# Kernel optimization log

Hardware: AMD Instinct MI355X
Metric: run time of the kernel (lower is better)

## Reference

```python
import jax, jax.numpy as jnp
import numpy as np

# ---- static config (matches init_kwargs / langevin args) ----
B, N, D = 2, 16384, 3
F_DIM = 128      # feature_net.out_channels
H_DIM = 128      # score_net hidden
N_BLOCKS = 2
K = 4            # denoise_knn
NUM_STEPS = 4
STEP_SIZE = 0.2
STEP_DECAY = 0.95

# static sliding-window neighbor indices, computed once (numpy -> constant)
_offsets = np.arange(-(K - 1) // 2, (K - 1) // 2 + 1)
NBR_IDX = np.clip(np.arange(N)[:, None] + _offsets, 0, N - 1)   # (N, K)
NBR_FLAT = NBR_IDX.reshape(-1)                                  # (N*K,)


def setup_inputs() -> dict:
    key = jax.random.key(0)
    ks = jax.random.split(key, 8)
    s = 0.05
    return {
        "pcl_noisy": jax.random.normal(ks[0], (B, N, D), jnp.float32),
        "Wf1": jax.random.normal(ks[1], (D, F_DIM), jnp.float32) * s,
        "bf1": jnp.zeros((F_DIM,), jnp.float32),
        "Wf2": jax.random.normal(ks[2], (F_DIM, F_DIM), jnp.float32) * s,
        "bf2": jnp.zeros((F_DIM,), jnp.float32),
        "W0": jax.random.normal(ks[3], (D + F_DIM, H_DIM), jnp.float32) * s,
        "b0": jnp.zeros((H_DIM,), jnp.float32),
        "Wb": jax.random.normal(ks[4], (N_BLOCKS, H_DIM, H_DIM), jnp.float32) * s,
        "bb": jnp.zeros((N_BLOCKS, H_DIM), jnp.float32),
        "Wo": jax.random.normal(ks[5], (H_DIM, D), jnp.float32) * s,
        "bo": jnp.zeros((D,), jnp.float32),
    }


def _feature_net(pcl, Wf1, bf1, Wf2, bf2):
    # pointwise MLP: (B,N,3) -> (B,N,F)
    h = jax.nn.relu(pcl @ Wf1 + bf1)
    return h @ Wf2 + bf2


def _score_net(x_cent, feat, W0, b0, Wb, bb, Wo, bo):
    # x_cent: (B,N,K,3) centered frames, feat: (B,N,F) per-seed context
    c = jnp.broadcast_to(feat[:, :, None, :], x_cent.shape[:3] + (feat.shape[-1],))
    h = jax.nn.relu(jnp.concatenate([x_cent, c], axis=-1) @ W0 + b0)  # (B,N,K,H)
    for i in range(N_BLOCKS):  # small fixed residual stack
        h = h + jax.nn.relu(h @ Wb[i] + bb[i])
    return h @ Wo + bo  # (B,N,K,3)


def reference(pcl_noisy, Wf1, bf1, Wf2, bf2, W0, b0, Wb, bb, Wo, bo):
    feat = _feature_net(pcl_noisy, Wf1, bf1, Wf2, bf2)  # (B,N,F), computed once

    def step(pcl_next, step_i):
        frames = pcl_next[:, NBR_IDX, :]                      # gather (B,N,K,3)
        centered = frames - pcl_noisy[:, :, None, :]          # center on original cloud
        grad_pred = _score_net(centered, feat, W0, b0, Wb, bb, Wo, bo)  # (B,N,K,3)
        acc = jnp.zeros_like(pcl_noisy).at[:, NBR_FLAT, :].add(
            grad_pred.reshape(pcl_noisy.shape[0], -1, D))     # scatter_add (B,N,3)
        s = STEP_SIZE * (STEP_DECAY ** step_i.astype(jnp.float32))
        return pcl_next + s * acc, None

    pcl_next, _ = jax.lax.scan(step, pcl_noisy, jnp.arange(NUM_STEPS))
    return pcl_next
```

## Files before the change

### kernel.cpp

```cpp
#include <hip/hip_runtime.h>
#include <hip/hip_bf16.h>

#define NPT    16384
#define TOTP   32768
#define FD     128
#define CHK    64
#define CPB    (NPT/CHK)
#define GRID   (2*CPB)
#define EXT    (CHK+24)
#define FQM    (CHK+21)

#define OFF_WFA 0
#define OFF_WFB 16384
#define OFF_WB  32768
#define OFF_WO  98304
#define PREP_TOT 100352

typedef unsigned short u16;
typedef __attribute__((ext_vector_type(8))) short bf16x8;
typedef __attribute__((ext_vector_type(4))) float f32x4;

__device__ __forceinline__ float bf2f(u16 u) {
    union { unsigned int i; float f; } v; v.i = ((unsigned int)u) << 16; return v.f;
}
__device__ __forceinline__ u16 f2bf(float f) {
    union { float f; unsigned int i; } v; v.f = f;
    unsigned int u = v.i;
    u = u + 0x7FFFu + ((u >> 16) & 1u);
    return (u16)(u >> 16);
}
__device__ __forceinline__ u16 f2bf_hw(float f) {
    __hip_bfloat16 h = __float2bfloat16(f);
    return *(u16*)&h;
}
__device__ __forceinline__ int swz(int row, int colbyte) {
    return row*256 + (colbyte ^ ((row & 7) << 4));
}
__device__ __forceinline__ int fswz(int row, int col) {
    return row*256 + ((col*2) ^ ((row & 7) << 4));
}

__global__ __launch_bounds__(256) void prep_weights(
    const float* __restrict__ Wf2, const float* __restrict__ W0,
    const float* __restrict__ Wb,  const float* __restrict__ Wo,
    u16* __restrict__ W)
{
    int t = blockIdx.x*256 + threadIdx.x;
    if (t >= PREP_TOT) return;
    float val;
    if (t < OFF_WB) {
        int u = t & 16383;
        int e = u & 7, l = (u >> 3) & 63, kk = (u >> 9) & 3;
        int ntg = (u >> 11) & 1, wid = (u >> 12) & 3;
        int col = wid*32 + ntg*16 + (l & 15);
        int k   = kk*32 + (l >> 4)*8 + e;
        val = (t < OFF_WFB) ? Wf2[k*FD + col] : W0[(3+k)*FD + col];
    } else if (t < OFF_WO) {
        int u = t - OFF_WB;
        int e = u & 7, l = (u >> 3) & 63, kk = (u >> 9) & 3;
        int ntg = (u >> 11) & 1, layer = (u >> 12) & 1, wid = (u >> 13) & 3;
        int col = wid*32 + ntg*16 + (l & 15);
        int k   = kk*32 + (l >> 4)*8 + e;
        val = Wb[layer*FD*FD + k*FD + col];
    } else {
        int u = t - OFF_WO;
        int e = u & 7, l = (u >> 3) & 63, kk = (u >> 9) & 3;
        int l15 = l & 15;
        int k   = kk*32 + (l >> 4)*8 + e;
        val = (l15 < 3) ? Wo[k*3 + l15] : 0.f;
    }
    W[t] = f2bf(val);
}

__global__ __launch_bounds__(256, 2) void fused_all(
    const float* __restrict__ pcl, const float* __restrict__ Wf1,
    const float* __restrict__ bf1, const float* __restrict__ bf2,
    const float* __restrict__ W0,  const float* __restrict__ b0,
    const float* __restrict__ bb,  const float* __restrict__ bo,
    const u16* __restrict__ Wprep, float* __restrict__ out)
{
    __shared__ __align__(16) u16   fpl[FQM*128];
    __shared__ __align__(16) float X0l[EXT*3];
    __shared__ __align__(16) float Xal[EXT*3];
    __shared__ __align__(16) float Xbl[EXT*3];
    __shared__ __align__(16) char  hA0[8192];
    __shared__ __align__(16) char  hA1[8192];
    __shared__ __align__(16) char  hB0[8192];
    __shared__ __align__(16) char  hB1[8192];
    __shared__ __align__(16) char  hC0[8192];
    __shared__ __align__(16) char  hC1[8192];

    const int tid = threadIdx.x, wid = tid >> 6, l = tid & 63;
    const int l15 = l & 15, l4 = l >> 4;
    const int colb = wid * 32;

    const int blk = blockIdx.x;
    const int b = blk >> 8, cidx = blk & (CPB - 1);
    const int A = cidx * CHK;
    const int Bp = A + CHK - 1;
    const int elo  = (A - 12 < 0) ? 0 : A - 12;
    const int ehi  = (Bp + 12 > NPT-1) ? NPT-1 : Bp + 12;
    const int esz3 = (ehi - elo + 1) * 3;
    const int fqlo = (A - 10 < 0) ? 0 : A - 10;
    const int fqhi = (Bp + 11 > NPT-1) ? NPT-1 : Bp + 11;
    const int fqc  = fqhi - fqlo + 1;
    const size_t gb = (size_t)b * NPT;

    for (int i = tid; i < esz3; i += 256) X0l[i] = pcl[(gb + elo)*3 + i];
    __syncthreads();

    {
        bf16x8 wfA[2][4], wfB[2][4];
        {
            const bf16x8* fa = (const bf16x8*)(Wprep + OFF_WFA);
            const bf16x8* fb = (const bf16x8*)(Wprep + OFF_WFB);
            #pragma unroll
            for (int ntg = 0; ntg < 2; ++ntg)
                #pragma unroll
                for (int kk = 0; kk < 4; ++kk) {
                    int fi = ((wid*2 + ntg)*4 + kk)*64 + l;
                    wfA[ntg][kk] = fa[fi];
                    wfB[ntg][kk] = fb[fi];
                }
        }
        float wf1c[3][2], bf1v[2], bf2v[2], b0v[2];
        #pragma unroll
        for (int ntg = 0; ntg < 2; ++ntg) {
            int col = colb + ntg*16 + l15;
            wf1c[0][ntg] = Wf1[0*FD+col];
            wf1c[1][ntg] = Wf1[1*FD+col];
            wf1c[2][ntg] = Wf1[2*FD+col];
            bf1v[ntg] = bf1[col]; bf2v[ntg] = bf2[col]; b0v[ntg] = b0[col];
        }
        const int nft = (fqc + 31) >> 5;
        for (int ft = 0; ft < nft; ++ft) {
            const int r0 = ft*32;
            #pragma unroll
            for (int rt = 0; rt < 2; ++rt)
                #pragma unroll
                for (int reg = 0; reg < 4; ++reg) {
                    int row = rt*16 + l4*4 + reg;
                    int q = fqlo + r0 + row; if (q > fqhi) q = fqhi;
                    int qe = (q - elo)*3;
                    float px = X0l[qe], py = X0l[qe+1], pz = X0l[qe+2];
                    #pragma unroll
                    for (int ntg = 0; ntg < 2; ++ntg) {
                        float tv = bf1v[ntg] + px*wf1c[0][ntg] + py*wf1c[1][ntg] + pz*wf1c[2][ntg];
                        tv = fmaxf(tv, 0.f);
                        int col = colb + ntg*16 + l15;
                        *(u16*)(hA0 + swz(row, col*2)) = f2bf_hw(tv);
                    }
                }
            __syncthreads();
            {
                bf16x8 a[2][4];
                #pragma unroll
                for (int rt = 0; rt < 2; ++rt)
                    #pragma unroll
                    for (int kk = 0; kk < 4; ++kk)
                        a[rt][kk] = *(const bf16x8*)(hA0 + swz(rt*16 + l15, kk*64 + l4*16));
                #pragma unroll
                for (int ntg = 0; ntg < 2; ++ntg) {
                    f32x4 acc0 = {bf2v[ntg],bf2v[ntg],bf2v[ntg],bf2v[ntg]};
                    f32x4 acc1 = acc0;
                    #pragma unroll
                    for (int kk = 0; kk < 4; ++kk) {
                        acc0 = __builtin_amdgcn_mfma_f32_16x16x32_bf16(a[0][kk], wfA[ntg][kk], acc0, 0,0,0);
                        acc1 = __builtin_amdgcn_mfma_f32_16x16x32_bf16(a[1][kk], wfA[ntg][kk], acc1, 0,0,0);
                    }
                    int col = colb + ntg*16 + l15;
                    #pragma unroll
                    for (int reg = 0; reg < 4; ++reg) {
                        *(u16*)(hB0 + swz(l4*4+reg,    col*2)) = f2bf_hw(acc0[reg]);
                        *(u16*)(hB0 + swz(16+l4*4+reg, col*2)) = f2bf_hw(acc1[reg]);
                    }
                }
            }
            __syncthreads();
            {
                bf16x8 a[2][4];
                #pragma unroll
                for (int rt = 0; rt < 2; ++rt)
                    #pragma unroll
                    for (int kk = 0; kk < 4; ++kk)
                        a[rt][kk] = *(const bf16x8*)(hB0 + swz(rt*16 + l15, kk*64 + l4*16));
                #pragma unroll
                for (int ntg = 0; ntg < 2; ++ntg) {
                    f32x4 acc0 = {b0v[ntg],b0v[ntg],b0v[ntg],b0v[ntg]};
                    f32x4 acc1 = acc0;
                    #pragma unroll
                    for (int kk = 0; kk < 4; ++kk) {
                        acc0 = __builtin_amdgcn_mfma_f32_16x16x32_bf16(a[0][kk], wfB[ntg][kk], acc0, 0,0,0);
                        acc1 = __builtin_amdgcn_mfma_f32_16x16x32_bf16(a[1][kk], wfB[ntg][kk], acc1, 0,0,0);
                    }
                    int col = colb + ntg*16 + l15;
                    #pragma unroll
                    for (int reg = 0; reg < 4; ++reg) {
                        int ra = r0 + l4*4 + reg, rb = r0 + 16 + l4*4 + reg;
                        if (ra < fqc) *(u16*)((char*)fpl + fswz(ra, col)) = f2bf_hw(acc0[reg]);
                        if (rb < fqc) *(u16*)((char*)fpl + fswz(rb, col)) = f2bf_hw(acc1[reg]);
                    }
                }
            }
            __syncthreads();
        }
    }
    __builtin_amdgcn_sched_barrier(0);

    bf16x8 wfrag[2][2][4], wofrag[4];
    {
        const bf16x8* wb = (const bf16x8*)(Wprep + OFF_WB);
        #pragma unroll
        for (int layer = 0; layer < 2; ++layer)
            #pragma unroll
            for (int ntg = 0; ntg < 2; ++ntg)
                #pragma unroll
                for (int kk = 0; kk < 4; ++kk)
                    wfrag[layer][ntg][kk] = wb[(((wid*2+layer)*2+ntg)*4+kk)*64 + l];
        const bf16x8* wo = (const bf16x8*)(Wprep + OFF_WO);
        #pragma unroll
        for (int kk = 0; kk < 4; ++kk) wofrag[kk] = wo[kk*64 + l];
    }
    float w0c[3][2], bbv[2][2];
    #pragma unroll
    for (int ntg = 0; ntg < 2; ++ntg) {
        int col = colb + ntg*16 + l15;
        w0c[0][ntg] = W0[0*FD+col];
        w0c[1][ntg] = W0[1*FD+col];
        w0c[2][ntg] = W0[2*FD+col];
        bbv[0][ntg] = bb[col]; bbv[1][ntg] = bb[FD+col];
    }
    const float bol = (l15 < 3) ? bo[l15] : 0.f;

    auto do_step = [&](const float* curl, float* nxtl, float sval, int qlo, int qhi) {
        for (int i = tid; i < esz3; i += 256) nxtl[i] = curl[i];
        __syncthreads();

        auto layer0 = [&](char* hAt, int qbase, float (&hc)[2][2][4]) {
            #pragma unroll
            for (int rt = 0; rt < 2; ++rt) {
                int q = qbase + rt*4 + l4; if (q > qhi) q = qhi;
                int qe = (q - elo)*3;
                float nx = X0l[qe], ny = X0l[qe+1], nz = X0l[qe+2];
                float cx[4], cy[4], cz[4];
                #pragma unroll
                for (int k = 0; k < 4; ++k) {
                    int nb = q + k - 2;
                    nb = nb < 0 ? 0 : (nb > NPT-1 ? NPT-1 : nb);
                    int te = (nb - elo)*3;
                    cx[k] = curl[te]   - nx;
                    cy[k] = curl[te+1] - ny;
                    cz[k] = curl[te+2] - nz;
                }
                #pragma unroll
                for (int ntg = 0; ntg < 2; ++ntg) {
                    int col = colb + ntg*16 + l15;
                    float fp = bf2f(*(const u16*)((const char*)fpl + fswz(q - fqlo, col)));
                    #pragma unroll
                    for (int reg = 0; reg < 4; ++reg) {
                        float u = fp + cx[reg]*w0c[0][ntg] + cy[reg]*w0c[1][ntg] + cz[reg]*w0c[2][ntg];
                        u = fmaxf(u, 0.f);
                        hc[rt][ntg][reg] = u;
                        *(u16*)(hAt + swz(rt*16 + l4*4 + reg, col*2)) = f2bf_hw(u);
                    }
                }
            }
        };
        auto layer1 = [&](const char* hAt, char* hBt, float (&hc)[2][2][4]) {
            bf16x8 a[2][4];
            #pragma unroll
            for (int rt = 0; rt < 2; ++rt)
                #pragma unroll
                for (int kk = 0; kk < 4; ++kk)
                    a[rt][kk] = *(const bf16x8*)(hAt + swz(rt*16 + l15, kk*64 + l4*16));
            #pragma unroll
            for (int ntg = 0; ntg < 2; ++ntg) {
                f32x4 acc0 = {bbv[0][ntg],bbv[0][ntg],bbv[0][ntg],bbv[0][ntg]};
                f32x4 acc1 = acc0;
                #pragma unroll
                for (int kk = 0; kk < 4; ++kk) {
                    acc0 = __builtin_amdgcn_mfma_f32_16x16x32_bf16(a[0][kk], wfrag[0][ntg][kk], acc0, 0,0,0);
                    acc1 = __builtin_amdgcn_mfma_f32_16x16x32_bf16(a[1][kk], wfrag[0][ntg][kk], acc1, 0,0,0);
                }
                int col = colb + ntg*16 + l15;
                #pragma unroll
                for (int reg = 0; reg < 4; ++reg) {
                    hc[0][ntg][reg] += fmaxf(acc0[reg], 0.f);
                    hc[1][ntg][reg] += fmaxf(acc1[reg], 0.f);
                    *(u16*)(hBt + swz(l4*4+reg,    col*2)) = f2bf_hw(hc[0][ntg][reg]);
                    *(u16*)(hBt + swz(16+l4*4+reg, col*2)) = f2bf_hw(hc[1][ntg][reg]);
                }
            }
        };
        auto layer2 = [&](const char* hBt, char* hCt, float (&hc)[2][2][4]) {
            bf16x8 a[2][4];
            #pragma unroll
            for (int rt = 0; rt < 2; ++rt)
                #pragma unroll
                for (int kk = 0; kk < 4; ++kk)
                    a[rt][kk] = *(const bf16x8*)(hBt + swz(rt*16 + l15, kk*64 + l4*16));
            #pragma unroll
            for (int ntg = 0; ntg < 2; ++ntg) {
                f32x4 acc0 = {bbv[1][ntg],bbv[1][ntg],bbv[1][ntg],bbv[1][ntg]};
                f32x4 acc1 = acc0;
                #pragma unroll
                for (int kk = 0; kk < 4; ++kk) {
                    acc0 = __builtin_amdgcn_mfma_f32_16x16x32_bf16(a[0][kk], wfrag[1][ntg][kk], acc0, 0,0,0);
                    acc1 = __builtin_amdgcn_mfma_f32_16x16x32_bf16(a[1][kk], wfrag[1][ntg][kk], acc1, 0,0,0);
                }
                int col = colb + ntg*16 + l15;
                #pragma unroll
                for (int reg = 0; reg < 4; ++reg) {
                    float h0 = hc[0][ntg][reg] + fmaxf(acc0[reg], 0.f);
                    float h1 = hc[1][ntg][reg] + fmaxf(acc1[reg], 0.f);
                    *(u16*)(hCt + swz(l4*4+reg,    col*2)) = f2bf_hw(h0);
                    *(u16*)(hCt + swz(16+l4*4+reg, col*2)) = f2bf_hw(h1);
                }
            }
        };

        const int nt_ = (qhi - qlo + 8) >> 3;
        const int ng_ = (nt_ + 1) >> 1;
        for (int g = 0; g < ng_; ++g) {
            const int qb0 = qlo + (g*2)*8;
            const int qb1 = qlo + (g*2+1)*8;
            const bool has1 = (g*2+1) < nt_;
            float hc0[2][2][4], hc1[2][2][4];
            layer0(hA0, qb0, hc0);
            if (has1) layer0(hA1, qb1, hc1);
            __syncthreads();
            layer1(hA0, hB0, hc0);
            if (has1) layer1(hA1, hB1, hc1);
            __syncthreads();
            layer2(hB0, hC0, hc0);
            if (has1) layer2(hB1, hC1, hc1);
            __syncthreads();
            {
                const int t = wid >> 1, sub = wid & 1;
                const char* hCt = t ? hC1 : hC0;
                const int qb = t ? qb1 : qb0;
                bf16x8 a[4];
                #pragma unroll
                for (int kk = 0; kk < 4; ++kk)
                    a[kk] = *(const bf16x8*)(hCt + swz(sub*16 + l15, kk*64 + l4*16));
                f32x4 acc = {0.f,0.f,0.f,0.f};
                #pragma unroll
                for (int kk = 0; kk < 4; ++kk)
                    acc = __builtin_amdgcn_mfma_f32_16x16x32_bf16(a[kk], wofrag[kk], acc, 0,0,0);
                int q = qb + sub*4 + l4;
                if (l15 < 3 && q <= qhi) {
                    #pragma unroll
                    for (int reg = 0; reg < 4; ++reg) {
                        int nb = q + reg - 2;
                        nb = nb < 0 ? 0 : (nb > NPT-1 ? NPT-1 : nb);
                        atomicAdd(&nxtl[(nb - elo)*3 + l15], sval*(acc[reg] + bol));
                    }
                }
            }
        }
        __syncthreads();
    };

    const int q1lo = fqlo,                 q1hi = fqhi;
    const int q2lo = (A-7 < 0) ? 0 : A-7,  q2hi = (Bp+8 > NPT-1) ? NPT-1 : Bp+8;
    const int q3lo = (A-4 < 0) ? 0 : A-4,  q3hi = (Bp+5 > NPT-1) ? NPT-1 : Bp+5;
    const int q4lo = (A-1 < 0) ? 0 : A-1,  q4hi = (Bp+2 > NPT-1) ? NPT-1 : Bp+2;

    do_step(X0l, Xal, 0.2f,      q1lo, q1hi);
    do_step(Xal, Xbl, 0.19f,     q2lo, q2hi);
    do_step(Xbl, Xal, 0.1805f,   q3lo, q3hi);
    do_step(Xal, Xbl, 0.171475f, q4lo, q4hi);

    for (int i = tid; i < CHK*3; i += 256)
        out[(gb + A)*3 + i] = Xbl[(A - elo)*3 + i];
}

extern "C" void kernel_launch(void* const* d_in, const int* in_sizes, int n_in,
                              void* d_out, int out_size, void* d_ws, size_t ws_size,
                              hipStream_t stream) {
    const float* pcl = (const float*)d_in[0];
    const float* Wf1 = (const float*)d_in[1];
    const float* bf1 = (const float*)d_in[2];
    const float* Wf2 = (const float*)d_in[3];
    const float* bf2 = (const float*)d_in[4];
    const float* W0  = (const float*)d_in[5];
    const float* b0  = (const float*)d_in[6];
    const float* Wb  = (const float*)d_in[7];
    const float* bb  = (const float*)d_in[8];
    const float* Wo  = (const float*)d_in[9];
    const float* bo  = (const float*)d_in[10];
    float* out = (float*)d_out;

    u16* Wprep = (u16*)d_ws;

    prep_weights<<<(PREP_TOT+255)/256, 256, 0, stream>>>(Wf2, W0, Wb, Wo, Wprep);
    fused_all<<<GRID, 256, 0, stream>>>(pcl, Wf1, bf1, bf2, W0, b0, bb, bo, Wprep, out);
}
```

Before: 174.5 us.

## Interleave activation tiles as packed bf16 pairs and pad point coords to float4

Changes the LDS activation layout so each 32-bit word holds the values for row r and row r+16, which lets each layer write packed u32 stores instead of 16-bit stores. Reads do two 16-byte loads followed by bit shuffles that rebuild the MFMA A fragments. Point-cloud buffers in LDS are padded to four floats per point so neighbour and center reads, step copies and atomics use float4 accesses. The aim is fewer, wider LDS transactions, at the cost of extra ALU work to unpack fragments and somewhat more LDS for coordinates.

Result: slower. 237.2 us (+35.9%).

```diff
diff --git a/kernel.cpp b/kernel.cpp
--- a/kernel.cpp
+++ b/kernel.cpp
@@ -17,6 +17,7 @@
 #define PREP_TOT 100352
 
 typedef unsigned short u16;
+typedef unsigned int   u32;
 typedef __attribute__((ext_vector_type(8))) short bf16x8;
 typedef __attribute__((ext_vector_type(4))) float f32x4;
 
@@ -33,8 +34,11 @@
     __hip_bfloat16 h = __float2bfloat16(f);
     return *(u16*)&h;
 }
-__device__ __forceinline__ int swz(int row, int colbyte) {
-    return row*256 + (colbyte ^ ((row & 7) << 4));
+__device__ __forceinline__ u32 pk2(float lo, float hi) {
+    return (u32)f2bf_hw(lo) | ((u32)f2bf_hw(hi) << 16);
+}
+__device__ __forceinline__ int hswz(int r15, int col) {
+    return r15*512 + ((col*4) ^ ((r15 & 7) << 4));
 }
 __device__ __forceinline__ int fswz(int row, int col) {
     return row*256 + ((col*2) ^ ((row & 7) << 4));
@@ -80,9 +84,9 @@
     const u16* __restrict__ Wprep, float* __restrict__ out)
 {
     __shared__ __align__(16) u16   fpl[FQM*128];
-    __shared__ __align__(16) float X0l[EXT*3];
-    __shared__ __align__(16) float Xal[EXT*3];
-    __shared__ __align__(16) float Xbl[EXT*3];
+    __shared__ __align__(16) float X0l[EXT*4];
+    __shared__ __align__(16) float Xal[EXT*4];
+    __shared__ __align__(16) float Xbl[EXT*4];
     __shared__ __align__(16) char  hA0[8192];
     __shared__ __align__(16) char  hA1[8192];
     __shared__ __align__(16) char  hB0[8192];
@@ -100,14 +104,41 @@
     const int Bp = A + CHK - 1;
     const int elo  = (A - 12 < 0) ? 0 : A - 12;
     const int ehi  = (Bp + 12 > NPT-1) ? NPT-1 : Bp + 12;
-    const int esz3 = (ehi - elo + 1) * 3;
+    const int extc = ehi - elo + 1;
     const int fqlo = (A - 10 < 0) ? 0 : A - 10;
     const int fqhi = (Bp + 11 > NPT-1) ? NPT-1 : Bp + 11;
     const int fqc  = fqhi - fqlo + 1;
     const size_t gb = (size_t)b * NPT;
 
-    for (int i = tid; i < esz3; i += 256) X0l[i] = pcl[(gb + elo)*3 + i];
+    for (int i = tid; i < extc; i += 256) {
+        float4 v;
+        v.x = pcl[(gb + elo + i)*3 + 0];
+        v.y = pcl[(gb + elo + i)*3 + 1];
+        v.z = pcl[(gb + elo + i)*3 + 2];
+        v.w = 0.f;
+        *(float4*)&X0l[i*4] = v;
+    }
     __syncthreads();
+
+    auto load_ab = [&](const char* hXt, bf16x8 (&a)[2][4]) {
+        #pragma unroll
+        for (int kk = 0; kk < 4; ++kk) {
+            int k0 = kk*32 + l4*8;
+            uint4 da = *(const uint4*)(hXt + hswz(l15, k0));
+            uint4 db = *(const uint4*)(hXt + hswz(l15, k0 + 4));
+            union { u32 u[4]; bf16x8 v; } u0, u1;
+            u0.u[0] = (da.x & 0xffffu) | (da.y << 16);
+            u0.u[1] = (da.z & 0xffffu) | (da.w << 16);
+            u0.u[2] = (db.x & 0xffffu) | (db.y << 16);
+            u0.u[3] = (db.z & 0xffffu) | (db.w << 16);
+            u1.u[0] = (da.x >> 16) | (da.y & 0xffff0000u);
+            u1.u[1] = (da.z >> 16) | (da.w & 0xffff0000u);
+            u1.u[2] = (db.x >> 16) | (db.y & 0xffff0000u);
+            u1.u[3] = (db.z >> 16) | (db.w & 0xffff0000u);
+            a[0][kk] = u0.v;
+            a[1][kk] = u1.v;
+        }
+    };
 
     {
         bf16x8 wfA[2][4], wfB[2][4];
@@ -135,30 +166,33 @@
         const int nft = (fqc + 31) >> 5;
         for (int ft = 0; ft < nft; ++ft) {
             const int r0 = ft*32;
-            #pragma unroll
-            for (int rt = 0; rt < 2; ++rt)
-                #pragma unroll
-                for (int reg = 0; reg < 4; ++reg) {
-                    int row = rt*16 + l4*4 + reg;
-                    int q = fqlo + r0 + row; if (q > fqhi) q = fqhi;
-                    int qe = (q - elo)*3;
-                    float px = X0l[qe], py = X0l[qe+1], pz = X0l[qe+2];
-                    #pragma unroll
-                    for (int ntg = 0; ntg < 2; ++ntg) {
-                        float tv = bf1v[ntg] + px*wf1c[0][ntg] + py*wf1c[1][ntg] + pz*wf1c[2][ntg];
-                        tv = fmaxf(tv, 0.f);
-                        int col = colb + ntg*16 + l15;
-                        *(u16*)(hA0 + swz(row, col*2)) = f2bf_hw(tv);
-                    }
-                }
+            {
+                float tvv[2][2][4];
+                #pragma unroll
+                for (int rt = 0; rt < 2; ++rt)
+                    #pragma unroll
+                    for (int reg = 0; reg < 4; ++reg) {
+                        int row = rt*16 + l4*4 + reg;
+                        int q = fqlo + r0 + row; if (q > fqhi) q = fqhi;
+                        float4 pv = *(const float4*)&X0l[(q - elo)*4];
+                        #pragma unroll
+                        for (int ntg = 0; ntg < 2; ++ntg) {
+                            float tv = bf1v[ntg] + pv.x*wf1c[0][ntg] + pv.y*wf1c[1][ntg] + pv.z*wf1c[2][ntg];
+                            tvv[rt][ntg][reg] = fmaxf(tv, 0.f);
+                        }
+                    }
+                #pragma unroll
+                for (int ntg = 0; ntg < 2; ++ntg) {
+                    int col = colb + ntg*16 + l15;
+                    #pragma unroll
+                    for (int reg = 0; reg < 4; ++reg)
+                        *(u32*)(hA0 + hswz(l4*4+reg, col)) = pk2(tvv[0][ntg][reg], tvv[1][ntg][reg]);
+                }
+            }
             __syncthreads();
             {
                 bf16x8 a[2][4];
-                #pragma unroll
-                for (int rt = 0; rt < 2; ++rt)
-                    #pragma unroll
-                    for (int kk = 0; kk < 4; ++kk)
-                        a[rt][kk] = *(const bf16x8*)(hA0 + swz(rt*16 + l15, kk*64 + l4*16));
+                load_ab(hA0, a);
                 #pragma unroll
                 for (int ntg = 0; ntg < 2; ++ntg) {
                     f32x4 acc0 = {bf2v[ntg],bf2v[ntg],bf2v[ntg],bf2v[ntg]};
@@ -170,20 +204,14 @@
                     }
                     int col = colb + ntg*16 + l15;
                     #pragma unroll
-                    for (int reg = 0; reg < 4; ++reg) {
-                        *(u16*)(hB0 + swz(l4*4+reg,    col*2)) = f2bf_hw(acc0[reg]);
-                        *(u16*)(hB0 + swz(16+l4*4+reg, col*2)) = f2bf_hw(acc1[reg]);
-                    }
+                    for (int reg = 0; reg < 4; ++reg)
+                        *(u32*)(hB0 + hswz(l4*4+reg, col)) = pk2(acc0[reg], acc1[reg]);
                 }
             }
             __syncthreads();
             {
                 bf16x8 a[2][4];
-                #pragma unroll
-                for (int rt = 0; rt < 2; ++rt)
-                    #pragma unroll
-                    for (int kk = 0; kk < 4; ++kk)
-                        a[rt][kk] = *(const bf16x8*)(hB0 + swz(rt*16 + l15, kk*64 + l4*16));
+                load_ab(hB0, a);
                 #pragma unroll
                 for (int ntg = 0; ntg < 2; ++ntg) {
                     f32x4 acc0 = {b0v[ntg],b0v[ntg],b0v[ntg],b0v[ntg]};
@@ -233,24 +261,24 @@
     const float bol = (l15 < 3) ? bo[l15] : 0.f;
 
     auto do_step = [&](const float* curl, float* nxtl, float sval, int qlo, int qhi) {
-        for (int i = tid; i < esz3; i += 256) nxtl[i] = curl[i];
+        for (int i = tid; i < extc; i += 256)
+            *(float4*)&nxtl[i*4] = *(const float4*)&curl[i*4];
         __syncthreads();
 
         auto layer0 = [&](char* hAt, int qbase, float (&hc)[2][2][4]) {
             #pragma unroll
             for (int rt = 0; rt < 2; ++rt) {
                 int q = qbase + rt*4 + l4; if (q > qhi) q = qhi;
-                int qe = (q - elo)*3;
-                float nx = X0l[qe], ny = X0l[qe+1], nz = X0l[qe+2];
+                float4 nv = *(const float4*)&X0l[(q - elo)*4];
                 float cx[4], cy[4], cz[4];
                 #pragma unroll
                 for (int k = 0; k < 4; ++k) {
                     int nb = q + k - 2;
                     nb = nb < 0 ? 0 : (nb > NPT-1 ? NPT-1 : nb);
-                    int te = (nb - elo)*3;
-                    cx[k] = curl[te]   - nx;
-                    cy[k] = curl[te+1] - ny;
-                    cz[k] = curl[te+2] - nz;
+                    float4 cv = *(const float4*)&curl[(nb - elo)*4];
+                    cx[k] = cv.x - nv.x;
+                    cy[k] = cv.y - nv.y;
+                    cz[k] = cv.z - nv.z;
                 }
                 #pragma unroll
                 for (int ntg = 0; ntg < 2; ++ntg) {
@@ -259,20 +287,21 @@
                     #pragma unroll
                     for (int reg = 0; reg < 4; ++reg) {
                         float u = fp + cx[reg]*w0c[0][ntg] + cy[reg]*w0c[1][ntg] + cz[reg]*w0c[2][ntg];
-                        u = fmaxf(u, 0.f);
-                        hc[rt][ntg][reg] = u;
-                        *(u16*)(hAt + swz(rt*16 + l4*4 + reg, col*2)) = f2bf_hw(u);
-                    }
-                }
+                        hc[rt][ntg][reg] = fmaxf(u, 0.f);
+                    }
+                }
+            }
+            #pragma unroll
+            for (int ntg = 0; ntg < 2; ++ntg) {
+                int col = colb + ntg*16 + l15;
+                #pragma unroll
+                for (int reg = 0; reg < 4; ++reg)
+                    *(u32*)(hAt + hswz(l4*4+reg, col)) = pk2(hc[0][ntg][reg], hc[1][ntg][reg]);
             }
         };
         auto layer1 = [&](const char* hAt, char* hBt, float (&hc)[2][2][4]) {
             bf16x8 a[2][4];
-            #pragma unroll
-            for (int rt = 0; rt < 2; ++rt)
-                #pragma unroll
-                for (int kk = 0; kk < 4; ++kk)
-                    a[rt][kk] = *(const bf16x8*)(hAt + swz(rt*16 + l15, kk*64 + l4*16));
+            load_ab(hAt, a);
             #pragma unroll
             for (int ntg = 0; ntg < 2; ++ntg) {
                 f32x4 acc0 = {bbv[0][ntg],bbv[0][ntg],bbv[0][ntg],bbv[0][ntg]};
@@ -287,18 +316,13 @@
                 for (int reg = 0; reg < 4; ++reg) {
                     hc[0][ntg][reg] += fmaxf(acc0[reg], 0.f);
                     hc[1][ntg][reg] += fmaxf(acc1[reg], 0.f);
-                    *(u16*)(hBt + swz(l4*4+reg,    col*2)) = f2bf_hw(hc[0][ntg][reg]);
-                    *(u16*)(hBt + swz(16+l4*4+reg, col*2)) = f2bf_hw(hc[1][ntg][reg]);
+                    *(u32*)(hBt + hswz(l4*4+reg, col)) = pk2(hc[0][ntg][reg], hc[1][ntg][reg]);
                 }
             }
         };
         auto layer2 = [&](const char* hBt, char* hCt, float (&hc)[2][2][4]) {
             bf16x8 a[2][4];
-            #pragma unroll
-            for (int rt = 0; rt < 2; ++rt)
-                #pragma unroll
-                for (int kk = 0; kk < 4; ++kk)
-                    a[rt][kk] = *(const bf16x8*)(hBt + swz(rt*16 + l15, kk*64 + l4*16));
+            load_ab(hBt, a);
             #pragma unroll
             for (int ntg = 0; ntg < 2; ++ntg) {
                 f32x4 acc0 = {bbv[1][ntg],bbv[1][ntg],bbv[1][ntg],bbv[1][ntg]};
@@ -313,8 +337,7 @@
                 for (int reg = 0; reg < 4; ++reg) {
                     float h0 = hc[0][ntg][reg] + fmaxf(acc0[reg], 0.f);
                     float h1 = hc[1][ntg][reg] + fmaxf(acc1[reg], 0.f);
-                    *(u16*)(hCt + swz(l4*4+reg,    col*2)) = f2bf_hw(h0);
-                    *(u16*)(hCt + swz(16+l4*4+reg, col*2)) = f2bf_hw(h1);
+                    *(u32*)(hCt + hswz(l4*4+reg, col)) = pk2(h0, h1);
                 }
             }
         };
@@ -341,8 +364,24 @@
                 const int qb = t ? qb1 : qb0;
                 bf16x8 a[4];
                 #pragma unroll
-                for (int kk = 0; kk < 4; ++kk)
-                    a[kk] = *(const bf16x8*)(hCt + swz(sub*16 + l15, kk*64 + l4*16));
+                for (int kk = 0; kk < 4; ++kk) {
+                    int k0 = kk*32 + l4*8;
+                    uint4 da = *(const uint4*)(hCt + hswz(l15, k0));
+                    uint4 db = *(const uint4*)(hCt + hswz(l15, k0 + 4));
+                    union { u32 u[4]; bf16x8 v; } ua;
+                    if (sub == 0) {
+                        ua.u[0] = (da.x & 0xffffu) | (da.y << 16);
+                        ua.u[1] = (da.z & 0xffffu) | (da.w << 16);
+                        ua.u[2] = (db.x & 0xffffu) | (db.y << 16);
+                        ua.u[3] = (db.z & 0xffffu) | (db.w << 16);
+                    } else {
+                        ua.u[0] = (da.x >> 16) | (da.y & 0xffff0000u);
+                        ua.u[1] = (da.z >> 16) | (da.w & 0xffff0000u);
+                        ua.u[2] = (db.x >> 16) | (db.y & 0xffff0000u);
+                        ua.u[3] = (db.z >> 16) | (db.w & 0xffff0000u);
+                    }
+                    a[kk] = ua.v;
+                }
                 f32x4 acc = {0.f,0.f,0.f,0.f};
                 #pragma unroll
                 for (int kk = 0; kk < 4; ++kk)
@@ -353,7 +392,7 @@
                     for (int reg = 0; reg < 4; ++reg) {
                         int nb = q + reg - 2;
                         nb = nb < 0 ? 0 : (nb > NPT-1 ? NPT-1 : nb);
-                        atomicAdd(&nxtl[(nb - elo)*3 + l15], sval*(acc[reg] + bol));
+                        atomicAdd(&nxtl[(nb - elo)*4 + l15], sval*(acc[reg] + bol));
                     }
                 }
             }
@@ -371,8 +410,10 @@
     do_step(Xbl, Xal, 0.1805f,   q3lo, q3hi);
     do_step(Xal, Xbl, 0.171475f, q4lo, q4hi);
 
-    for (int i = tid; i < CHK*3; i += 256)
-        out[(gb + A)*3 + i] = Xbl[(A - elo)*3 + i];
+    for (int i = tid; i < CHK*3; i += 256) {
+        int row = i / 3, c = i - row*3;
+        out[(gb + A)*3 + i] = Xbl[(A - elo + row)*4 + c];
+    }
 }
 
 extern "C" void kernel_launch(void* const* d_in, const int* in_sizes, int n_in,
```
